# Performance work log

Measured on AMD Instinct MI355X. Metric: run time of the kernel, lower is better.

Reference implementation:

```python
import jax, jax.numpy as jnp
import numpy as np

LMAX = 3
D_IN = 16    # sum(2l+1) for l=0..3
D_OUT = 156  # sum over the 34 CG instructions of (2*l3+1)


def _build_sparse_cg():
    """Build the concatenated sparse CG index lists (mu1, mu2, mu3) and
    coefficients, mirroring TensorProduct.__init__: loop over all
    (l1, l2, l3) paths with l3 <= LMAX, take nonzeros of the real-basis
    Wigner-3j tensor (nonzero pattern: |m1' +- m2'| == |m3'|), offset the
    indices by the per-irrep block offsets, and concatenate.
    Coefficient values are deterministic synthetic stand-ins with the
    correct sparsity structure and component-normalization scale."""
    rs = np.random.RandomState(0)
    off_in = [0, 1, 4, 9]  # block offsets for l = 0..3 (block dim 2l+1)
    mu1, mu2, mu3, vals = [], [], [], []
    off3 = 0
    for l1 in range(LMAX + 1):
        for l2 in range(LMAX + 1):
            for l3 in range(abs(l1 - l2), min(l1 + l2, LMAX) + 1):
                for m1 in range(2 * l1 + 1):
                    for m2 in range(2 * l2 + 1):
                        a, b = m1 - l1, m2 - l2
                        for m3 in range(2 * l3 + 1):
                            c = m3 - l3
                            if abs(a + b) == abs(c) or abs(a - b) == abs(c):
                                mu1.append(off_in[l1] + m1)
                                mu2.append(off_in[l2] + m2)
                                mu3.append(off3 + m3)
                                vals.append(rs.randn() / np.sqrt(2 * l3 + 1))
                off3 += 2 * l3 + 1
    assert off3 == D_OUT
    return (np.asarray(mu1, np.int32), np.asarray(mu2, np.int32),
            np.asarray(mu3, np.int32), np.asarray(vals, np.float32))


def setup_inputs() -> dict:
    key = jax.random.key(0)
    k1, k2 = jax.random.split(key)
    B, C = 1024, 128
    x = jax.random.normal(k1, (B, D_IN, C), dtype=jnp.float32)
    y = jax.random.normal(k2, (B, D_IN, C), dtype=jnp.float32)
    mu1, mu2, mu3, cg = _build_sparse_cg()
    return {
        "x": x,
        "y": y,
        "cg": jnp.asarray(cg),
        "mu1": jnp.asarray(mu1),
        "mu2": jnp.asarray(mu2),
        "mu3": jnp.asarray(mu3),
    }


def reference(x, y, cg, mu1, mu2, mu3):
    # Fused equivalent of the per-batch / per-instruction Python loops:
    # out[b, mu3[k], c] += cg[k] * x[b, mu1[k], c] * y[b, mu2[k], c]
    terms = x[:, mu1, :] * cg[None, :, None] * y[:, mu2, :]  # [B, K, C]
    out = jnp.zeros((x.shape[0], D_OUT, x.shape[2]), dtype=x.dtype)
    return out.at[:, mu3, :].add(terms)
```

## Files before the change

### kernel.cpp

```cpp
#include <hip/hip_runtime.h>
#include <utility>


#define D_IN_ 16
#define D_OUT_ 156
#define C_ 128
#define KMAX_ 2048

struct CGRows {
    int n;
    int start[D_OUT_ + 1];
    int k[KMAX_];
    int m1[KMAX_];
    int m2[KMAX_];
};

constexpr CGRows build_rows() {
    int mu1[KMAX_] = {}, mu2[KMAX_] = {}, mu3[KMAX_] = {};
    int n = 0;
    const int off_in[4] = {0, 1, 4, 9};
    int off3 = 0;
    for (int l1 = 0; l1 <= 3; ++l1) {
        for (int l2 = 0; l2 <= 3; ++l2) {
            int lo = l1 > l2 ? l1 - l2 : l2 - l1;
            int hi = (l1 + l2) < 3 ? (l1 + l2) : 3;
            for (int l3 = lo; l3 <= hi; ++l3) {
                for (int m1 = 0; m1 < 2 * l1 + 1; ++m1) {
                    for (int m2 = 0; m2 < 2 * l2 + 1; ++m2) {
                        int a = m1 - l1, b = m2 - l2;
                        for (int m3 = 0; m3 < 2 * l3 + 1; ++m3) {
                            int c = m3 - l3;
                            int s = a + b; if (s < 0) s = -s;
                            int d = a - b; if (d < 0) d = -d;
                            int e = c < 0 ? -c : c;
                            if (s == e || d == e) {
                                mu1[n] = off_in[l1] + m1;
                                mu2[n] = off_in[l2] + m2;
                                mu3[n] = off3 + m3;
                                ++n;
                            }
                        }
                    }
                }
                off3 += 2 * l3 + 1;
            }
        }
    }
    CGRows r{};
    r.n = n;
    int cnt[D_OUT_] = {};
    for (int i = 0; i < n; ++i) cnt[mu3[i]]++;
    r.start[0] = 0;
    for (int j = 0; j < D_OUT_; ++j) r.start[j + 1] = r.start[j] + cnt[j];
    int pos[D_OUT_] = {};
    for (int j = 0; j < D_OUT_; ++j) pos[j] = r.start[j];
    for (int i = 0; i < n; ++i) {
        int j = mu3[i];
        int p = pos[j]++;
        r.k[p] = i;
        r.m1[p] = mu1[i];
        r.m2[p] = mu2[i];
    }
    return r;
}

constexpr CGRows CG = build_rows();
constexpr int K = CG.n;
static_assert(K <= KMAX_, "KMAX too small");

constexpr int findq(int i) {
    int target = (CG.n * i) / 4;
    int j = 0;
    while (CG.start[j] < target) ++j;
    return j;
}
constexpr int QS0 = 0, QS1 = findq(1), QS2 = findq(2), QS3 = findq(3), QS4 = D_OUT_;

constexpr unsigned need1(int j0, int j1) {
    unsigned m = 0;
    for (int p = CG.start[j0]; p < CG.start[j1]; ++p) m |= 1u << CG.m1[p];
    return m;
}
constexpr unsigned need2(int j0, int j1) {
    unsigned m = 0;
    for (int p = CG.start[j0]; p < CG.start[j1]; ++p) m |= 1u << CG.m2[p];
    return m;
}

__device__ __constant__ CGRows dCG = build_rows();

__global__ void gather_cg(const float* __restrict__ cg, float* __restrict__ cgs) {
    int i = blockIdx.x * 256 + threadIdx.x;
    if (i < K) cgs[i] = cg[dCG.k[i]];
}

template <unsigned M, int I>
__device__ __forceinline__ void load1(float (&v)[D_IN_], const float* __restrict__ base) {
    if constexpr ((M >> I) & 1u) v[I] = base[I * C_];
    else v[I] = 0.0f;
}

template <unsigned M, int... Is>
__device__ __forceinline__ void load_masked(float (&v)[D_IN_], const float* __restrict__ base,
                                            std::integer_sequence<int, Is...>) {
    (load1<M, Is>(v, base), ...);
}

template <int Base, int... Ts>
__device__ __forceinline__ float row_sum(const float* __restrict__ cgs,
                                         const float (&xv)[D_IN_],
                                         const float (&yv)[D_IN_],
                                         std::integer_sequence<int, Ts...>) {
    float s = 0.0f;
    ((s = fmaf(cgs[Base + Ts], xv[CG.m1[Base + Ts]] * yv[CG.m2[Base + Ts]], s)), ...);
    return s;
}

template <int J>
__device__ __forceinline__ void store_row(float* __restrict__ ob, const float* __restrict__ cgs,
                                          const float (&xv)[D_IN_], const float (&yv)[D_IN_]) {
    constexpr int base = CG.start[J];
    constexpr int nt = CG.start[J + 1] - CG.start[J];
    ob[J * C_] = row_sum<base>(cgs, xv, yv, std::make_integer_sequence<int, nt>{});
}

template <int J0, int... Js>
__device__ __forceinline__ void rows_range(float* __restrict__ ob, const float* __restrict__ cgs,
                                           const float (&xv)[D_IN_], const float (&yv)[D_IN_],
                                           std::integer_sequence<int, Js...>) {
    (store_row<J0 + Js>(ob, cgs, xv, yv), ...);
}

template <int J0, int J1>
__device__ __forceinline__ void do_range(const float* __restrict__ xb,
                                         const float* __restrict__ yb,
                                         float* __restrict__ ob,
                                         const float* __restrict__ cgs) {
    constexpr unsigned M1 = need1(J0, J1), M2 = need2(J0, J1);
    float xv[D_IN_], yv[D_IN_];
    load_masked<M1>(xv, xb, std::make_integer_sequence<int, D_IN_>{});
    load_masked<M2>(yv, yb, std::make_integer_sequence<int, D_IN_>{});
    rows_range<J0>(ob, cgs, xv, yv, std::make_integer_sequence<int, J1 - J0>{});
}

__global__ __launch_bounds__(256, 4) void tp_cg_kernel(
    const float* __restrict__ x, const float* __restrict__ y,
    const float* __restrict__ cgs, float* __restrict__ out) {
    const int tid = (int)threadIdx.x;
    const int c = tid & (C_ - 1);
    const int b = (int)(blockIdx.x >> 1);
    const int q = (int)(((blockIdx.x & 1) << 1) | (tid >> 7));

    const float* xb = x + (size_t)b * (D_IN_ * C_) + c;
    const float* yb = y + (size_t)b * (D_IN_ * C_) + c;
    float* ob = out + (size_t)b * (D_OUT_ * C_) + c;

    if (q == 0)      do_range<QS0, QS1>(xb, yb, ob, cgs);
    else if (q == 1) do_range<QS1, QS2>(xb, yb, ob, cgs);
    else if (q == 2) do_range<QS2, QS3>(xb, yb, ob, cgs);
    else             do_range<QS3, QS4>(xb, yb, ob, cgs);
}

extern "C" void kernel_launch(void* const* d_in, const int* in_sizes, int n_in,
                              void* d_out, int out_size, void* d_ws, size_t ws_size,
                              hipStream_t stream) {
    const float* x  = (const float*)d_in[0];
    const float* y  = (const float*)d_in[1];
    const float* cg = (const float*)d_in[2];
    float* out = (float*)d_out;
    float* cgs = (float*)d_ws;

    const int B = in_sizes[0] / (D_IN_ * C_);

    gather_cg<<<(K + 255) / 256, 256, 0, stream>>>(cg, cgs);

    tp_cg_kernel<<<B * 2, 256, 0, stream>>>(x, y, cgs, out);
}
```

Before: 112.5 us.

## Split CG rows into eighths and loop phases inside each block

Result: no change. 113.1 us (+0.6%).

```diff
diff --git a/kernel.cpp b/kernel.cpp
--- a/kernel.cpp
+++ b/kernel.cpp
@@ -68,13 +68,15 @@
 constexpr int K = CG.n;
 static_assert(K <= KMAX_, "KMAX too small");
 
-constexpr int findq(int i) {
-    int target = (CG.n * i) / 4;
+constexpr int findo(int i) {
+    int target = (CG.n * i) / 8;
     int j = 0;
     while (CG.start[j] < target) ++j;
     return j;
 }
-constexpr int QS0 = 0, QS1 = findq(1), QS2 = findq(2), QS3 = findq(3), QS4 = D_OUT_;
+constexpr int OB0 = 0, OB1 = findo(1), OB2 = findo(2), OB3 = findo(3),
+              OB4 = findo(4), OB5 = findo(5), OB6 = findo(6), OB7 = findo(7),
+              OB8 = D_OUT_;
 
 constexpr unsigned need1(int j0, int j1) {
     unsigned m = 0;
@@ -145,20 +147,33 @@
 
 __global__ __launch_bounds__(256, 4) void tp_cg_kernel(
     const float* __restrict__ x, const float* __restrict__ y,
-    const float* __restrict__ cgs, float* __restrict__ out) {
+    const float* __restrict__ cgs, float* __restrict__ out, int B) {
     const int tid = (int)threadIdx.x;
     const int c = tid & (C_ - 1);
-    const int b = (int)(blockIdx.x >> 1);
-    const int q = (int)(((blockIdx.x & 1) << 1) | (tid >> 7));
+    const int qhalf = tid >> 7;
 
-    const float* xb = x + (size_t)b * (D_IN_ * C_) + c;
-    const float* yb = y + (size_t)b * (D_IN_ * C_) + c;
-    float* ob = out + (size_t)b * (D_OUT_ * C_) + c;
+#pragma unroll 1
+    for (int p = 0; p < 4; ++p) {
+#pragma unroll 1
+        for (int b = (int)blockIdx.x; b < B; b += (int)gridDim.x) {
+            const int oct = (p << 1) | qhalf;
 
-    if (q == 0)      do_range<QS0, QS1>(xb, yb, ob, cgs);
-    else if (q == 1) do_range<QS1, QS2>(xb, yb, ob, cgs);
-    else if (q == 2) do_range<QS2, QS3>(xb, yb, ob, cgs);
-    else             do_range<QS3, QS4>(xb, yb, ob, cgs);
+            const float* xb = x + (size_t)b * (D_IN_ * C_) + c;
+            const float* yb = y + (size_t)b * (D_IN_ * C_) + c;
+            float* ob = out + (size_t)b * (D_OUT_ * C_) + c;
+
+            switch (oct) {
+                case 0: do_range<OB0, OB1>(xb, yb, ob, cgs); break;
+                case 1: do_range<OB1, OB2>(xb, yb, ob, cgs); break;
+                case 2: do_range<OB2, OB3>(xb, yb, ob, cgs); break;
+                case 3: do_range<OB3, OB4>(xb, yb, ob, cgs); break;
+                case 4: do_range<OB4, OB5>(xb, yb, ob, cgs); break;
+                case 5: do_range<OB5, OB6>(xb, yb, ob, cgs); break;
+                case 6: do_range<OB6, OB7>(xb, yb, ob, cgs); break;
+                default: do_range<OB7, OB8>(xb, yb, ob, cgs); break;
+            }
+        }
+    }
 }
 
 extern "C" void kernel_launch(void* const* d_in, const int* in_sizes, int n_in,
@@ -174,5 +189,5 @@
 
     gather_cg<<<(K + 255) / 256, 256, 0, stream>>>(cg, cgs);
 
-    tp_cg_kernel<<<B * 2, 256, 0, stream>>>(x, y, cgs, out);
+    tp_cg_kernel<<<B, 256, 0, stream>>>(x, y, cgs, out, B);
 }
```
